# Kernel optimization log

Hardware: AMD Instinct MI355X
Metric: run time of the kernel (lower is better)

Reference implementation:

```python
import jax, jax.numpy as jnp
import numpy as np

N = 27          # num_classes (nodes)
C = 512         # in_channels
B = 64          # batch
EPS = 1e-5


def _bn(x, gamma, beta):
    # BatchNorm1d over [b, channels, feat]: normalize over (batch, feat), training mode (batch stats, biased var)
    mean = jnp.mean(x, axis=(0, 2), keepdims=True)
    var = jnp.mean((x - mean) ** 2, axis=(0, 2), keepdims=True)
    return gamma[None, :, None] * (x - mean) * jax.lax.rsqrt(var + EPS) + beta[None, :, None]


def _layer(x, edge, WA, WB, WE, WU, WV, ge, be, gv, bv):
    # x: [b, n, c], edge: [b, n*n, c]; edge index e = i*n + j; end[e,i]=1, start[e,j]=1
    b = x.shape[0]
    res = x
    Vix = x @ WA.T                       # [b, n, c]  (gathered to edges via end)
    Vjx = x @ WB.T                       # [b, n, c]  (gathered to edges via start)
    e_lin = edge @ WE.T                  # [b, n*n, c]
    # einsum('ev,bvc->bec', end, Vix) == broadcast Vix over j; start gathers Vjx over i
    msg = (Vix[:, :, None, :] + Vjx[:, None, :, :]).reshape(b, N * N, C) + e_lin
    edge = edge + jax.nn.relu(_bn(msg, ge, be))
    # attention: sigmoid then softmax over j (dim 2 of [b, n, n, c])
    e = jax.nn.sigmoid(edge).reshape(b, N, N, C)
    e = jax.nn.softmax(e, axis=2).reshape(b, N * N, C)
    Ujx = x @ WV.T                       # [b, n, c], gathered via start -> broadcast over i
    Ujx_e = jnp.broadcast_to(Ujx[:, None, :, :], (b, N, N, C)).reshape(b, N * N, C)
    Uix = x @ WU.T
    # einsum('ve,bec->bvc', end.T, t) == sum over j of t[b, i*n+j]
    agg = (e * Ujx_e).reshape(b, N, N, C).sum(axis=2)
    x = Uix + agg / N
    x = jax.nn.relu(res + _bn(x, gv, bv))
    return x, edge


def setup_inputs() -> dict:
    key = jax.random.key(0)
    ks = jax.random.split(key, 12)
    scale = np.sqrt(2.0 / C)
    w = lambda k: (jax.random.normal(k, (C, C), dtype=jnp.float32) * scale)
    inp = {
        "x": jax.random.normal(ks[0], (B, N, C), dtype=jnp.float32),
        "edge": jax.random.normal(ks[1], (B, N * N, C), dtype=jnp.float32),
        "WU1": w(ks[2]), "WV1": w(ks[3]), "WA1": w(ks[4]), "WB1": w(ks[5]), "WE1": w(ks[6]),
        "WU2": w(ks[7]), "WV2": w(ks[8]), "WA2": w(ks[9]), "WB2": w(ks[10]), "WE2": w(ks[11]),
        "gv1": jnp.ones((N,), jnp.float32), "bv1": jnp.zeros((N,), jnp.float32),
        "ge1": jnp.ones((N * N,), jnp.float32), "be1": jnp.zeros((N * N,), jnp.float32),
        "gv2": jnp.ones((N,), jnp.float32), "bv2": jnp.zeros((N,), jnp.float32),
        "ge2": jnp.ones((N * N,), jnp.float32), "be2": jnp.zeros((N * N,), jnp.float32),
    }
    return inp


def reference(x, edge, WU1, WV1, WA1, WB1, WE1, WU2, WV2, WA2, WB2, WE2,
              gv1, bv1, ge1, be1, gv2, bv2, ge2, be2):
    x, edge = _layer(x, edge, WA1, WB1, WE1, WU1, WV1, ge1, be1, gv1, bv1)
    x, edge = _layer(x, edge, WA2, WB2, WE2, WU2, WV2, ge2, be2, gv2, bv2)
    return x, edge
```

## Files before the change

kernel.cpp:

```cpp
#include <hip/hip_runtime.h>

typedef unsigned short u16;
typedef unsigned int u32;
typedef __bf16 bf16x8 __attribute__((ext_vector_type(8)));
typedef float f32x4 __attribute__((ext_vector_type(4)));

#define DI __device__ __forceinline__

DI u16 f2bf(float f) {
  union { float f; u32 u; } v; v.f = f;
  return (u16)((v.u + 0x7fffu + ((v.u >> 16) & 1u)) >> 16);
}
DI float bf2f(u16 h) {
  union { u32 u; float f; } v; v.u = ((u32)h) << 16;
  return v.f;
}

DI void gload_lds16(const void* g, void* l) {
  __builtin_amdgcn_global_load_lds((const __attribute__((address_space(1))) u32*)g,
                                   (__attribute__((address_space(3))) u32*)l, 16, 0, 0);
}

constexpr float INV_M = 1.0f / 32768.0f;

__global__ void convw_k(const float* wa1, const float* wb1, const float* wu1, const float* wv1, const float* we1,
                        const float* wa2, const float* wb2, const float* wu2, const float* wv2, const float* we2,
                        u16* dst) {
  int idx = blockIdx.x * 256 + threadIdx.x;
  int m = idx >> 16;
  int i = (idx & 0xffff) << 2;
  const float* s;
  switch (m) {
    case 0: s = wa1; break; case 1: s = wb1; break; case 2: s = wu1; break;
    case 3: s = wv1; break; case 4: s = we1; break; case 5: s = wa2; break;
    case 6: s = wb2; break; case 7: s = wu2; break; case 8: s = wv2; break;
    default: s = we2; break;
  }
  float4 v = *(const float4*)(s + i);
  ushort4 o;
  o.x = f2bf(v.x); o.y = f2bf(v.y); o.z = f2bf(v.z); o.w = f2bf(v.w);
  *(ushort4*)(dst + ((size_t)m << 18) + i) = o;
}

template<int EPI, int ABF, int SWZ, int NT>
__global__ __launch_bounds__(256, 5) void gemm_k(
    const void* __restrict__ A_, const u16* __restrict__ W,
    float* __restrict__ outf, int ldout,
    u16* __restrict__ msg, const float* __restrict__ V4,
    float* __restrict__ esum, float* __restrict__ esq) {
  __shared__ __align__(16) u16 lA[64 * 64];
  __shared__ __align__(16) u16 lW[32 * NT * 64];
  const int tid = threadIdx.x;
  const int lane = tid & 63, wid = tid >> 6;
  const int wm = wid >> 1, wn = wid & 1;
  const int q = lane >> 4, l15 = lane & 15;
  const int lrow8 = lane >> 3, lg = lane & 7;

  int rb, cb;
  if (SWZ) {
    int l = blockIdx.x;
    int xcd = l & 7, t = l >> 3;
    cb = t & 3;
    rb = ((t >> 2) << 3) | xcd;
    if (rb >= 729) return;
  } else {
    rb = blockIdx.y; cb = blockIdx.x;
  }

  f32x4 acc[2][NT];
#pragma unroll
  for (int a = 0; a < 2; a++)
#pragma unroll
    for (int b = 0; b < NT; b++) acc[a][b] = (f32x4){0.f, 0.f, 0.f, 0.f};

  for (int k0 = 0; k0 < 512; k0 += 64) {
    __syncthreads();
    if (ABF) {
#pragma unroll
      for (int it = 0; it < 2; it++) {
        int ch = wid * 2 + it;
        int row = ch * 8 + lrow8;
        const u16* src = (const u16*)A_ + (((size_t)(rb * 64 + row)) << 9) + k0 + ((lg ^ (row & 7)) << 3);
        gload_lds16(src, lA + ch * 512);
      }
    } else {
#pragma unroll
      for (int s = tid; s < 512; s += 256) {
        int row = s >> 3, g = s & 7;
        const float* src = (const float*)A_ + (((size_t)(rb * 64 + row)) << 9) + k0 + g * 8;
        float4 s0 = *(const float4*)src;
        float4 s1 = *(const float4*)(src + 4);
        uint4 p;
        p.x = f2bf(s0.x) | ((u32)f2bf(s0.y) << 16);
        p.y = f2bf(s0.z) | ((u32)f2bf(s0.w) << 16);
        p.z = f2bf(s1.x) | ((u32)f2bf(s1.y) << 16);
        p.w = f2bf(s1.z) | ((u32)f2bf(s1.w) << 16);
        *(uint4*)(lA + row * 64 + ((g ^ (row & 7)) << 3)) = p;
      }
    }
#pragma unroll
    for (int it = 0; it < NT; it++) {
      int ch = wid * NT + it;
      int row = ch * 8 + lrow8;
      const u16* src = W + (((size_t)(cb * 32 * NT + row)) << 9) + k0 + ((lg ^ (row & 7)) << 3);
      gload_lds16(src, lW + ch * 512);
    }
    __syncthreads();
#pragma unroll
    for (int ks = 0; ks < 2; ks++) {
      const int gk = ks * 4 + q;
      bf16x8 af[2], wf[NT];
#pragma unroll
      for (int mt = 0; mt < 2; mt++) {
        int r = wm * 32 + mt * 16 + l15;
        af[mt] = *(const bf16x8*)(lA + r * 64 + ((gk ^ (r & 7)) << 3));
      }
#pragma unroll
      for (int nt = 0; nt < NT; nt++) {
        int r = wn * 16 * NT + nt * 16 + l15;
        wf[nt] = *(const bf16x8*)(lW + r * 64 + ((gk ^ (r & 7)) << 3));
      }
#pragma unroll
      for (int mt = 0; mt < 2; mt++)
#pragma unroll
        for (int nt = 0; nt < NT; nt++)
          acc[mt][nt] = __builtin_amdgcn_mfma_f32_16x16x32_bf16(af[mt], wf[nt], acc[mt][nt], 0, 0, 0);
    }
  }

  if (EPI == 1) {
#pragma unroll
    for (int mt = 0; mt < 2; mt++) {
      int grow0 = rb * 64 + wm * 32 + mt * 16 + q * 4;
#pragma unroll
      for (int nt = 0; nt < NT; nt++) {
        int gcol = cb * 32 * NT + wn * 16 * NT + nt * 16 + l15;
#pragma unroll
        for (int r = 0; r < 4; r++)
          outf[(size_t)(grow0 + r) * ldout + gcol] = acc[mt][nt][r];
      }
    }
  } else {
    float ms[2][4], m2[2][4];
#pragma unroll
    for (int mt = 0; mt < 2; mt++) {
#pragma unroll
      for (int r = 0; r < 4; r++) {
        int grow = rb * 64 + wm * 32 + mt * 16 + q * 4 + r;
        int b = grow / 729;
        int e = grow - b * 729;
        int i = e / 27;
        int j = e - i * 27;
        const float* vix = V4 + (((size_t)(b * 27 + i)) << 11);
        const float* vjx = V4 + (((size_t)(b * 27 + j)) << 11) + 512;
        u16* mrow = msg + (((size_t)grow) << 9);
        float s1 = 0.f, s2 = 0.f;
#pragma unroll
        for (int nt = 0; nt < NT; nt++) {
          int c = cb * 32 * NT + wn * 16 * NT + nt * 16 + l15;
          float m = acc[mt][nt][r] + vix[c] + vjx[c];
          mrow[c] = f2bf(m);
          s1 += m;
          s2 += m * m;
        }
        ms[mt][r] = s1;
        m2[mt][r] = s2;
      }
    }
#pragma unroll
    for (int msk = 1; msk < 16; msk <<= 1) {
#pragma unroll
      for (int mt = 0; mt < 2; mt++)
#pragma unroll
        for (int r = 0; r < 4; r++) {
          ms[mt][r] += __shfl_xor(ms[mt][r], msk);
          m2[mt][r] += __shfl_xor(m2[mt][r], msk);
        }
    }
    __syncthreads();
    float* sm = (float*)lA;
    if (l15 == 0) {
#pragma unroll
      for (int mt = 0; mt < 2; mt++)
#pragma unroll
        for (int r = 0; r < 4; r++) {
          int rib = wm * 32 + mt * 16 + q * 4 + r;
          sm[wn * 64 + rib] = ms[mt][r];
          sm[128 + wn * 64 + rib] = m2[mt][r];
        }
    }
    __syncthreads();
    if (tid < 64) {
      int grow = rb * 64 + tid;
      int e = grow % 729;
      atomicAdd(&esum[e], sm[tid] + sm[64 + tid]);
      atomicAdd(&esq[e], sm[128 + tid] + sm[192 + tid]);
    }
  }
}

template<int INBF, int OUTBF>
__global__ __launch_bounds__(256) void edge_attn_k(
    const u16* __restrict__ msg, const void* __restrict__ ein_, void* __restrict__ eout_,
    const float* __restrict__ esum, const float* __restrict__ esq,
    const float* __restrict__ ge, const float* __restrict__ be,
    const float* __restrict__ V4,
    float* __restrict__ xnew, float* __restrict__ vsum, float* __restrict__ vsq) {
  const int bi = blockIdx.x;
  const int b = bi / 27, i = bi - b * 27;
  const int t = threadIdx.x;
  __shared__ float2 sab[27];
  if (t < 27) {
    int e = i * 27 + t;
    float mean = esum[e] * INV_M;
    float var = esq[e] * INV_M - mean * mean;
    float a = ge[e] * rsqrtf(var + 1e-5f);
    sab[t] = make_float2(a, be[e] - mean * a);
  }
  __syncthreads();
  const size_t ebase = (((size_t)(b * 729 + i * 27)) << 9) + 2 * t;
  const u16* einb = (const u16*)ein_;
  const float* einf = (const float*)ein_;
  u16* eoutb = (u16*)eout_;
  float* eoutf = (float*)eout_;
  float t0[27], t1[27];
  float ss0 = 0.f, ss1 = 0.f;
#pragma unroll
  for (int j = 0; j < 27; j++) {
    size_t idx = ebase + (((size_t)j) << 9);
    float2 ab = sab[j];
    u32 mp = *(const u32*)(msg + idx);
    float2 ei;
    if (INBF) {
      u32 ep = *(const u32*)(einb + idx);
      ei = make_float2(bf2f((u16)ep), bf2f((u16)(ep >> 16)));
    } else {
      ei = *(const float2*)(einf + idx);
    }
    float e0 = ei.x + fmaxf(fmaf(ab.x, bf2f((u16)mp), ab.y), 0.f);
    float e1 = ei.y + fmaxf(fmaf(ab.x, bf2f((u16)(mp >> 16)), ab.y), 0.f);
    if (OUTBF) {
      *(u32*)(eoutb + idx) = (u32)f2bf(e0) | ((u32)f2bf(e1) << 16);
    } else {
      *(float2*)(eoutf + idx) = make_float2(e0, e1);
    }
    float x0 = __expf(1.f / (1.f + __expf(-e0)));
    float x1 = __expf(1.f / (1.f + __expf(-e1)));
    ss0 += x0; ss1 += x1;
    t0[j] = x0; t1[j] = x1;
  }
  float a0 = 0.f, a1 = 0.f;
#pragma unroll
  for (int j = 0; j < 27; j++) {
    float2 uj = *(const float2*)(V4 + (((size_t)(b * 27 + j)) << 11) + 1536 + 2 * t);
    a0 = fmaf(t0[j], uj.x, a0);
    a1 = fmaf(t1[j], uj.y, a1);
  }
  float2 ui = *(const float2*)(V4 + (((size_t)(b * 27 + i)) << 11) + 1024 + 2 * t);
  float xn0 = ui.x + a0 / (ss0 * 27.f);
  float xn1 = ui.y + a1 / (ss1 * 27.f);
  *(float2*)(xnew + (((size_t)bi) << 9) + 2 * t) = make_float2(xn0, xn1);
  float v = xn0 + xn1, v2 = xn0 * xn0 + xn1 * xn1;
#pragma unroll
  for (int m = 32; m >= 1; m >>= 1) {
    v += __shfl_xor(v, m);
    v2 += __shfl_xor(v2, m);
  }
  __shared__ float red[8];
  int w = t >> 6, ln = t & 63;
  if (ln == 0) { red[w] = v; red[4 + w] = v2; }
  __syncthreads();
  if (t == 0) {
    float s1 = 0.f, s2 = 0.f;
#pragma unroll
    for (int k = 0; k < 4; k++) { s1 += red[k]; s2 += red[4 + k]; }
    atomicAdd(&vsum[i], s1);
    atomicAdd(&vsq[i], s2);
  }
}

__global__ void vert_bn_k(const float4* __restrict__ xnew, const float4* __restrict__ res,
                          const float* __restrict__ vsum, const float* __restrict__ vsq,
                          const float* __restrict__ g, const float* __restrict__ bt,
                          float4* __restrict__ out) {
  int idx = blockIdx.x * 256 + threadIdx.x;
  int i = (idx >> 7) % 27;
  float mean = vsum[i] * INV_M;
  float var = vsq[i] * INV_M - mean * mean;
  float a = g[i] * rsqrtf(var + 1e-5f);
  float bb = bt[i] - mean * a;
  float4 xv = xnew[idx];
  float4 rv = res[idx];
  float4 o;
  o.x = fmaxf(rv.x + fmaf(a, xv.x, bb), 0.f);
  o.y = fmaxf(rv.y + fmaf(a, xv.y, bb), 0.f);
  o.z = fmaxf(rv.z + fmaf(a, xv.z, bb), 0.f);
  o.w = fmaxf(rv.w + fmaf(a, xv.w, bb), 0.f);
  out[idx] = o;
}

extern "C" void kernel_launch(void* const* d_in, const int* in_sizes, int n_in,
                              void* d_out, int out_size, void* d_ws, size_t ws_size,
                              hipStream_t stream) {
  const float* x    = (const float*)d_in[0];
  const float* edge = (const float*)d_in[1];
  const float* WU1 = (const float*)d_in[2];
  const float* WV1 = (const float*)d_in[3];
  const float* WA1 = (const float*)d_in[4];
  const float* WB1 = (const float*)d_in[5];
  const float* WE1 = (const float*)d_in[6];
  const float* WU2 = (const float*)d_in[7];
  const float* WV2 = (const float*)d_in[8];
  const float* WA2 = (const float*)d_in[9];
  const float* WB2 = (const float*)d_in[10];
  const float* WE2 = (const float*)d_in[11];
  const float* gv1 = (const float*)d_in[12];
  const float* bv1 = (const float*)d_in[13];
  const float* ge1 = (const float*)d_in[14];
  const float* be1 = (const float*)d_in[15];
  const float* gv2 = (const float*)d_in[16];
  const float* bv2 = (const float*)d_in[17];
  const float* ge2 = (const float*)d_in[18];
  const float* be2 = (const float*)d_in[19];

  char* ws = (char*)d_ws;
  u16*   wbf  = (u16*)(ws + 0);
  float* V4   = (float*)(ws + 5242880);
  u16*   M1   = (u16*)(ws + 19398656);
  u16*   M2   = (u16*)(ws + 67174400);
  float* xnew = (float*)(ws + 114950144);
  float* x1   = (float*)(ws + 118489088);
  float* st   = (float*)(ws + 122028032);
  float* es1 = st;         float* eq1 = st + 729;
  float* es2 = st + 1458;  float* eq2 = st + 2187;
  float* vs1 = st + 2916;  float* vq1 = st + 2943;
  float* vs2 = st + 2970;  float* vq2 = st + 2997;

  float* xout = (float*)d_out;
  float* eo   = (float*)d_out + 884736;

  hipMemsetAsync(st, 0, 3024 * sizeof(float), stream);
  convw_k<<<dim3(2560), dim3(256), 0, stream>>>(WA1, WB1, WU1, WV1, WE1, WA2, WB2, WU2, WV2, WE2, wbf);

  gemm_k<1, 0, 0, 2><<<dim3(32, 27), dim3(256), 0, stream>>>(x, wbf, V4, 2048, nullptr, nullptr, nullptr, nullptr);
  gemm_k<2, 0, 1, 4><<<dim3(2944), dim3(256), 0, stream>>>(edge, wbf + 4 * 262144, nullptr, 0, M1, V4, es1, eq1);
  edge_attn_k<0, 1><<<dim3(1728), dim3(256), 0, stream>>>(M1, edge, M1, es1, eq1, ge1, be1, V4, xnew, vs1, vq1);
  vert_bn_k<<<dim3(864), dim3(256), 0, stream>>>((const float4*)xnew, (const float4*)x, vs1, vq1, gv1, bv1, (float4*)x1);

  gemm_k<1, 0, 0, 2><<<dim3(32, 27), dim3(256), 0, stream>>>(x1, wbf + 5 * 262144, V4, 2048, nullptr, nullptr, nullptr, nullptr);
  gemm_k<2, 1, 1, 4><<<dim3(2944), dim3(256), 0, stream>>>(M1, wbf + 9 * 262144, nullptr, 0, M2, V4, es2, eq2);
  edge_attn_k<1, 0><<<dim3(1728), dim3(256), 0, stream>>>(M2, M1, eo, es2, eq2, ge2, be2, V4, xnew, vs2, vq2);
  vert_bn_k<<<dim3(864), dim3(256), 0, stream>>>((const float4*)xnew, (const float4*)x1, vs2, vq2, gv2, bv2, (float4*)xout);
}
```

Baseline: 442.0 us.

## Replace LDS-staged GEMM with direct register-fragment loads and prefetch

The GEMM kernel no longer stages A and W tiles through shared memory. Each wave now loads its MFMA fragments straight from global memory into registers and double-buffers them, prefetching the next k-slice while the current MFMAs run. Every wave owns a 32x64 sub-tile, and the vertex GEMM grid is halved to match a 128-column block. This removes the LDS traffic and the per-k-step barriers, but each wave fetches its own copy of data that other waves share, with less coalesced global access and more register pressure.

```diff
diff --git a/kernel.cpp b/kernel.cpp
--- a/kernel.cpp
+++ b/kernel.cpp
@@ -15,10 +15,13 @@
   union { u32 u; float f; } v; v.u = ((u32)h) << 16;
   return v.f;
 }
-
-DI void gload_lds16(const void* g, void* l) {
-  __builtin_amdgcn_global_load_lds((const __attribute__((address_space(1))) u32*)g,
-                                   (__attribute__((address_space(3))) u32*)l, 16, 0, 0);
+DI bf16x8 pack8(float4 a, float4 b) {
+  union { bf16x8 v; u32 u[4]; } r;
+  r.u[0] = (u32)f2bf(a.x) | ((u32)f2bf(a.y) << 16);
+  r.u[1] = (u32)f2bf(a.z) | ((u32)f2bf(a.w) << 16);
+  r.u[2] = (u32)f2bf(b.x) | ((u32)f2bf(b.y) << 16);
+  r.u[3] = (u32)f2bf(b.z) | ((u32)f2bf(b.w) << 16);
+  return r.v;
 }
 
 constexpr float INV_M = 1.0f / 32768.0f;
@@ -42,20 +45,16 @@
   *(ushort4*)(dst + ((size_t)m << 18) + i) = o;
 }
 
-template<int EPI, int ABF, int SWZ, int NT>
-__global__ __launch_bounds__(256, 5) void gemm_k(
+template<int EPI, int ABF, int SWZ>
+__global__ __launch_bounds__(256, 4) void gemm_k(
     const void* __restrict__ A_, const u16* __restrict__ W,
     float* __restrict__ outf, int ldout,
     u16* __restrict__ msg, const float* __restrict__ V4,
     float* __restrict__ esum, float* __restrict__ esq) {
-  __shared__ __align__(16) u16 lA[64 * 64];
-  __shared__ __align__(16) u16 lW[32 * NT * 64];
   const int tid = threadIdx.x;
   const int lane = tid & 63, wid = tid >> 6;
-  const int wm = wid >> 1, wn = wid & 1;
+  const int vm = wid & 1, vn = wid >> 1;
   const int q = lane >> 4, l15 = lane & 15;
-  const int lrow8 = lane >> 3, lg = lane & 7;
-
   int rb, cb;
   if (SWZ) {
     int l = blockIdx.x;
@@ -67,86 +66,92 @@
     rb = blockIdx.y; cb = blockIdx.x;
   }
 
-  f32x4 acc[2][NT];
+  const u16*   wp0 = W + ((size_t)(cb * 128 + vn * 64 + l15) << 9) + q * 8;
+  const u16*   ab0 = (const u16*)A_  + ((size_t)(rb * 64 + vm * 32 + l15) << 9) + q * 8;
+  const float* af0 = (const float*)A_ + ((size_t)(rb * 64 + vm * 32 + l15) << 9) + q * 8;
+
+  f32x4 acc[2][4];
 #pragma unroll
   for (int a = 0; a < 2; a++)
 #pragma unroll
-    for (int b = 0; b < NT; b++) acc[a][b] = (f32x4){0.f, 0.f, 0.f, 0.f};
-
-  for (int k0 = 0; k0 < 512; k0 += 64) {
-    __syncthreads();
-    if (ABF) {
-#pragma unroll
-      for (int it = 0; it < 2; it++) {
-        int ch = wid * 2 + it;
-        int row = ch * 8 + lrow8;
-        const u16* src = (const u16*)A_ + (((size_t)(rb * 64 + row)) << 9) + k0 + ((lg ^ (row & 7)) << 3);
-        gload_lds16(src, lA + ch * 512);
+    for (int b = 0; b < 4; b++) acc[a][b] = (f32x4){0.f, 0.f, 0.f, 0.f};
+
+  bf16x8 wc[4], wn_[4];
+  bf16x8 ac[2], an_[2];
+  float4 fc[2][2], fn[2][2];
+
+#pragma unroll
+  for (int nt = 0; nt < 4; nt++) wc[nt] = *(const bf16x8*)(wp0 + nt * 8192);
+  if (ABF) {
+#pragma unroll
+    for (int mt = 0; mt < 2; mt++) ac[mt] = *(const bf16x8*)(ab0 + mt * 8192);
+  } else {
+#pragma unroll
+    for (int mt = 0; mt < 2; mt++) {
+      fc[mt][0] = *(const float4*)(af0 + mt * 8192);
+      fc[mt][1] = *(const float4*)(af0 + mt * 8192 + 4);
+    }
+  }
+
+#pragma unroll
+  for (int ks = 0; ks < 16; ks++) {
+    if (ks < 15) {
+      const int ko = (ks + 1) * 32;
+#pragma unroll
+      for (int nt = 0; nt < 4; nt++) wn_[nt] = *(const bf16x8*)(wp0 + nt * 8192 + ko);
+      if (ABF) {
+#pragma unroll
+        for (int mt = 0; mt < 2; mt++) an_[mt] = *(const bf16x8*)(ab0 + mt * 8192 + ko);
+      } else {
+#pragma unroll
+        for (int mt = 0; mt < 2; mt++) {
+          fn[mt][0] = *(const float4*)(af0 + mt * 8192 + ko);
+          fn[mt][1] = *(const float4*)(af0 + mt * 8192 + ko + 4);
+        }
       }
-    } else {
-#pragma unroll
-      for (int s = tid; s < 512; s += 256) {
-        int row = s >> 3, g = s & 7;
-        const float* src = (const float*)A_ + (((size_t)(rb * 64 + row)) << 9) + k0 + g * 8;
-        float4 s0 = *(const float4*)src;
-        float4 s1 = *(const float4*)(src + 4);
-        uint4 p;
-        p.x = f2bf(s0.x) | ((u32)f2bf(s0.y) << 16);
-        p.y = f2bf(s0.z) | ((u32)f2bf(s0.w) << 16);
-        p.z = f2bf(s1.x) | ((u32)f2bf(s1.y) << 16);
-        p.w = f2bf(s1.z) | ((u32)f2bf(s1.w) << 16);
-        *(uint4*)(lA + row * 64 + ((g ^ (row & 7)) << 3)) = p;
+    }
+    bf16x8 afr[2];
+#pragma unroll
+    for (int mt = 0; mt < 2; mt++)
+      afr[mt] = ABF ? ac[mt] : pack8(fc[mt][0], fc[mt][1]);
+#pragma unroll
+    for (int mt = 0; mt < 2; mt++)
+#pragma unroll
+      for (int nt = 0; nt < 4; nt++)
+        acc[mt][nt] = __builtin_amdgcn_mfma_f32_16x16x32_bf16(afr[mt], wc[nt], acc[mt][nt], 0, 0, 0);
+    if (ks < 15) {
+#pragma unroll
+      for (int nt = 0; nt < 4; nt++) wc[nt] = wn_[nt];
+      if (ABF) {
+#pragma unroll
+        for (int mt = 0; mt < 2; mt++) ac[mt] = an_[mt];
+      } else {
+#pragma unroll
+        for (int mt = 0; mt < 2; mt++) { fc[mt][0] = fn[mt][0]; fc[mt][1] = fn[mt][1]; }
       }
     }
-#pragma unroll
-    for (int it = 0; it < NT; it++) {
-      int ch = wid * NT + it;
-      int row = ch * 8 + lrow8;
-      const u16* src = W + (((size_t)(cb * 32 * NT + row)) << 9) + k0 + ((lg ^ (row & 7)) << 3);
-      gload_lds16(src, lW + ch * 512);
-    }
-    __syncthreads();
-#pragma unroll
-    for (int ks = 0; ks < 2; ks++) {
-      const int gk = ks * 4 + q;
-      bf16x8 af[2], wf[NT];
-#pragma unroll
-      for (int mt = 0; mt < 2; mt++) {
-        int r = wm * 32 + mt * 16 + l15;
-        af[mt] = *(const bf16x8*)(lA + r * 64 + ((gk ^ (r & 7)) << 3));
-      }
-#pragma unroll
-      for (int nt = 0; nt < NT; nt++) {
-        int r = wn * 16 * NT + nt * 16 + l15;
-        wf[nt] = *(const bf16x8*)(lW + r * 64 + ((gk ^ (r & 7)) << 3));
-      }
-#pragma unroll
-      for (int mt = 0; mt < 2; mt++)
-#pragma unroll
-        for (int nt = 0; nt < NT; nt++)
-          acc[mt][nt] = __builtin_amdgcn_mfma_f32_16x16x32_bf16(af[mt], wf[nt], acc[mt][nt], 0, 0, 0);
-    }
   }
 
   if (EPI == 1) {
 #pragma unroll
     for (int mt = 0; mt < 2; mt++) {
-      int grow0 = rb * 64 + wm * 32 + mt * 16 + q * 4;
-#pragma unroll
-      for (int nt = 0; nt < NT; nt++) {
-        int gcol = cb * 32 * NT + wn * 16 * NT + nt * 16 + l15;
+      int grow0 = rb * 64 + vm * 32 + mt * 16 + q * 4;
+#pragma unroll
+      for (int nt = 0; nt < 4; nt++) {
+        int gcol = cb * 128 + vn * 64 + nt * 16 + l15;
 #pragma unroll
         for (int r = 0; r < 4; r++)
           outf[(size_t)(grow0 + r) * ldout + gcol] = acc[mt][nt][r];
       }
     }
   } else {
+    __shared__ float sm[256];
     float ms[2][4], m2[2][4];
 #pragma unroll
     for (int mt = 0; mt < 2; mt++) {
 #pragma unroll
       for (int r = 0; r < 4; r++) {
-        int grow = rb * 64 + wm * 32 + mt * 16 + q * 4 + r;
+        int grow = rb * 64 + vm * 32 + mt * 16 + q * 4 + r;
         int b = grow / 729;
         int e = grow - b * 729;
         int i = e / 27;
@@ -156,8 +161,8 @@
         u16* mrow = msg + (((size_t)grow) << 9);
         float s1 = 0.f, s2 = 0.f;
 #pragma unroll
-        for (int nt = 0; nt < NT; nt++) {
-          int c = cb * 32 * NT + wn * 16 * NT + nt * 16 + l15;
+        for (int nt = 0; nt < 4; nt++) {
+          int c = cb * 128 + vn * 64 + nt * 16 + l15;
           float m = acc[mt][nt][r] + vix[c] + vjx[c];
           mrow[c] = f2bf(m);
           s1 += m;
@@ -178,15 +183,14 @@
         }
     }
     __syncthreads();
-    float* sm = (float*)lA;
     if (l15 == 0) {
 #pragma unroll
       for (int mt = 0; mt < 2; mt++)
 #pragma unroll
         for (int r = 0; r < 4; r++) {
-          int rib = wm * 32 + mt * 16 + q * 4 + r;
-          sm[wn * 64 + rib] = ms[mt][r];
-          sm[128 + wn * 64 + rib] = m2[mt][r];
+          int rib = vm * 32 + mt * 16 + q * 4 + r;
+          sm[vn * 64 + rib] = ms[mt][r];
+          sm[128 + vn * 64 + rib] = m2[mt][r];
         }
     }
     __syncthreads();
@@ -342,13 +346,13 @@
   hipMemsetAsync(st, 0, 3024 * sizeof(float), stream);
   convw_k<<<dim3(2560), dim3(256), 0, stream>>>(WA1, WB1, WU1, WV1, WE1, WA2, WB2, WU2, WV2, WE2, wbf);
 
-  gemm_k<1, 0, 0, 2><<<dim3(32, 27), dim3(256), 0, stream>>>(x, wbf, V4, 2048, nullptr, nullptr, nullptr, nullptr);
-  gemm_k<2, 0, 1, 4><<<dim3(2944), dim3(256), 0, stream>>>(edge, wbf + 4 * 262144, nullptr, 0, M1, V4, es1, eq1);
+  gemm_k<1, 0, 0><<<dim3(16, 27), dim3(256), 0, stream>>>(x, wbf, V4, 2048, nullptr, nullptr, nullptr, nullptr);
+  gemm_k<2, 0, 1><<<dim3(2944), dim3(256), 0, stream>>>(edge, wbf + 4 * 262144, nullptr, 0, M1, V4, es1, eq1);
   edge_attn_k<0, 1><<<dim3(1728), dim3(256), 0, stream>>>(M1, edge, M1, es1, eq1, ge1, be1, V4, xnew, vs1, vq1);
   vert_bn_k<<<dim3(864), dim3(256), 0, stream>>>((const float4*)xnew, (const float4*)x, vs1, vq1, gv1, bv1, (float4*)x1);
 
-  gemm_k<1, 0, 0, 2><<<dim3(32, 27), dim3(256), 0, stream>>>(x1, wbf + 5 * 262144, V4, 2048, nullptr, nullptr, nullptr, nullptr);
-  gemm_k<2, 1, 1, 4><<<dim3(2944), dim3(256), 0, stream>>>(M1, wbf + 9 * 262144, nullptr, 0, M2, V4, es2, eq2);
+  gemm_k<1, 0, 0><<<dim3(16, 27), dim3(256), 0, stream>>>(x1, wbf + 5 * 262144, V4, 2048, nullptr, nullptr, nullptr, nullptr);
+  gemm_k<2, 1, 1><<<dim3(2944), dim3(256), 0, stream>>>(M1, wbf + 9 * 262144, nullptr, 0, M2, V4, es2, eq2);
   edge_attn_k<1, 0><<<dim3(1728), dim3(256), 0, stream>>>(M2, M1, eo, es2, eq2, ge2, be2, V4, xnew, vs2, vq2);
   vert_bn_k<<<dim3(864), dim3(256), 0, stream>>>((const float4*)xnew, (const float4*)x1, vs2, vq2, gv2, bv2, (float4*)xout);
 }
```

After: 668.1 us. +51.1%, slower.

## Double-buffer weight tiles and register-prefetch A tiles in GEMM main loop

Applied to the files above, without the earlier changes.

Restructures the GEMM K-loop into a software pipeline. The next K-tile of W is loaded asynchronously into a second LDS buffer, and the next A tile is prefetched into registers while the MFMAs run on the current tile. The A registers are written to LDS after a barrier. This hides global-load latency behind compute, at the cost of extra LDS and registers, so launch bounds drop from 5 to 4 blocks per CU. The bf16 A path now also goes through registers instead of direct global-to-LDS loads.

```diff
diff --git a/kernel.cpp b/kernel.cpp
--- a/kernel.cpp
+++ b/kernel.cpp
@@ -43,18 +43,19 @@
 }
 
 template<int EPI, int ABF, int SWZ, int NT>
-__global__ __launch_bounds__(256, 5) void gemm_k(
+__global__ __launch_bounds__(256, 4) void gemm_k(
     const void* __restrict__ A_, const u16* __restrict__ W,
     float* __restrict__ outf, int ldout,
     u16* __restrict__ msg, const float* __restrict__ V4,
     float* __restrict__ esum, float* __restrict__ esq) {
   __shared__ __align__(16) u16 lA[64 * 64];
-  __shared__ __align__(16) u16 lW[32 * NT * 64];
+  __shared__ __align__(16) u16 lW[2][32 * NT * 64];
   const int tid = threadIdx.x;
   const int lane = tid & 63, wid = tid >> 6;
   const int wm = wid >> 1, wn = wid & 1;
   const int q = lane >> 4, l15 = lane & 15;
   const int lrow8 = lane >> 3, lg = lane & 7;
+  const int arow = tid >> 3, ag = tid & 7;
 
   int rb, cb;
   if (SWZ) {
@@ -67,45 +68,72 @@
     rb = blockIdx.y; cb = blockIdx.x;
   }
 
+  float4 pAf[2][2];
+  uint4 pAb[2];
+
+#define ISSUE_W(buf, k0)                                                                            \
+  {                                                                                                 \
+    _Pragma("unroll")                                                                               \
+    for (int it = 0; it < NT; it++) {                                                               \
+      int ch = wid * NT + it;                                                                       \
+      int row = ch * 8 + lrow8;                                                                     \
+      const u16* src = W + (((size_t)(cb * 32 * NT + row)) << 9) + (k0) + ((lg ^ (row & 7)) << 3);  \
+      gload_lds16(src, &lW[buf][ch * 512]);                                                         \
+    }                                                                                               \
+  }
+
+#define LOAD_A(k0)                                                                                  \
+  {                                                                                                 \
+    if (ABF) {                                                                                      \
+      _Pragma("unroll")                                                                             \
+      for (int i = 0; i < 2; i++)                                                                   \
+        pAb[i] = *(const uint4*)((const u16*)A_ + (((size_t)(rb * 64 + arow + 32 * i)) << 9) + (k0) + (ag << 3)); \
+    } else {                                                                                        \
+      _Pragma("unroll")                                                                             \
+      for (int i = 0; i < 2; i++) {                                                                 \
+        const float* s = (const float*)A_ + (((size_t)(rb * 64 + arow + 32 * i)) << 9) + (k0) + (ag << 3); \
+        pAf[i][0] = *(const float4*)s;                                                              \
+        pAf[i][1] = *(const float4*)(s + 4);                                                        \
+      }                                                                                             \
+    }                                                                                               \
+  }
+
+#define WRITE_A()                                                                                   \
+  {                                                                                                 \
+    _Pragma("unroll")                                                                               \
+    for (int i = 0; i < 2; i++) {                                                                   \
+      int row = arow + 32 * i;                                                                      \
+      uint4 p;                                                                                      \
+      if (ABF) {                                                                                    \
+        p = pAb[i];                                                                                 \
+      } else {                                                                                      \
+        p.x = f2bf(pAf[i][0].x) | ((u32)f2bf(pAf[i][0].y) << 16);                                   \
+        p.y = f2bf(pAf[i][0].z) | ((u32)f2bf(pAf[i][0].w) << 16);                                   \
+        p.z = f2bf(pAf[i][1].x) | ((u32)f2bf(pAf[i][1].y) << 16);                                   \
+        p.w = f2bf(pAf[i][1].z) | ((u32)f2bf(pAf[i][1].w) << 16);                                   \
+      }                                                                                             \
+      *(uint4*)(lA + row * 64 + ((ag ^ (row & 7)) << 3)) = p;                                       \
+    }                                                                                               \
+  }
+
   f32x4 acc[2][NT];
 #pragma unroll
   for (int a = 0; a < 2; a++)
 #pragma unroll
     for (int b = 0; b < NT; b++) acc[a][b] = (f32x4){0.f, 0.f, 0.f, 0.f};
 
-  for (int k0 = 0; k0 < 512; k0 += 64) {
+  LOAD_A(0);
+  ISSUE_W(0, 0);
+  WRITE_A();
+
+#pragma unroll 2
+  for (int kt = 0; kt < 8; kt++) {
     __syncthreads();
-    if (ABF) {
-#pragma unroll
-      for (int it = 0; it < 2; it++) {
-        int ch = wid * 2 + it;
-        int row = ch * 8 + lrow8;
-        const u16* src = (const u16*)A_ + (((size_t)(rb * 64 + row)) << 9) + k0 + ((lg ^ (row & 7)) << 3);
-        gload_lds16(src, lA + ch * 512);
-      }
-    } else {
-#pragma unroll
-      for (int s = tid; s < 512; s += 256) {
-        int row = s >> 3, g = s & 7;
-        const float* src = (const float*)A_ + (((size_t)(rb * 64 + row)) << 9) + k0 + g * 8;
-        float4 s0 = *(const float4*)src;
-        float4 s1 = *(const float4*)(src + 4);
-        uint4 p;
-        p.x = f2bf(s0.x) | ((u32)f2bf(s0.y) << 16);
-        p.y = f2bf(s0.z) | ((u32)f2bf(s0.w) << 16);
-        p.z = f2bf(s1.x) | ((u32)f2bf(s1.y) << 16);
-        p.w = f2bf(s1.z) | ((u32)f2bf(s1.w) << 16);
-        *(uint4*)(lA + row * 64 + ((g ^ (row & 7)) << 3)) = p;
-      }
-    }
-#pragma unroll
-    for (int it = 0; it < NT; it++) {
-      int ch = wid * NT + it;
-      int row = ch * 8 + lrow8;
-      const u16* src = W + (((size_t)(cb * 32 * NT + row)) << 9) + k0 + ((lg ^ (row & 7)) << 3);
-      gload_lds16(src, lW + ch * 512);
-    }
-    __syncthreads();
+    if (kt < 7) {
+      ISSUE_W((kt + 1) & 1, (kt + 1) * 64);
+      LOAD_A((kt + 1) * 64);
+    }
+    const u16* lWc = lW[kt & 1];
 #pragma unroll
     for (int ks = 0; ks < 2; ks++) {
       const int gk = ks * 4 + q;
@@ -118,7 +146,7 @@
 #pragma unroll
       for (int nt = 0; nt < NT; nt++) {
         int r = wn * 16 * NT + nt * 16 + l15;
-        wf[nt] = *(const bf16x8*)(lW + r * 64 + ((gk ^ (r & 7)) << 3));
+        wf[nt] = *(const bf16x8*)(lWc + r * 64 + ((gk ^ (r & 7)) << 3));
       }
 #pragma unroll
       for (int mt = 0; mt < 2; mt++)
@@ -126,6 +154,8 @@
         for (int nt = 0; nt < NT; nt++)
           acc[mt][nt] = __builtin_amdgcn_mfma_f32_16x16x32_bf16(af[mt], wf[nt], acc[mt][nt], 0, 0, 0);
     }
+    __syncthreads();
+    if (kt < 7) WRITE_A();
   }
 
   if (EPI == 1) {
```

New measurement: 432.3 us. -2.2%, faster.

## Double-buffer GEMM tiles via register prefetch and split edge attention over channels

Applied to the files above, without the earlier changes.

The GEMM drops direct global-to-LDS loads in favour of register-staged prefetch two k-tiles ahead into double-buffered LDS, with one barrier per k-step, so global loads overlap MFMA work. Occupancy hint drops from 5 to 3 waves because of the higher register and LDS use. The node GEMM switches to NT=4 with half the column blocks. Edge attention launches twice as many blocks, each thread handling one channel instead of two, which raises parallelism but makes memory accesses narrower.

```diff
diff --git a/kernel.cpp b/kernel.cpp
--- a/kernel.cpp
+++ b/kernel.cpp
@@ -15,10 +15,13 @@
   union { u32 u; float f; } v; v.u = ((u32)h) << 16;
   return v.f;
 }
-
-DI void gload_lds16(const void* g, void* l) {
-  __builtin_amdgcn_global_load_lds((const __attribute__((address_space(1))) u32*)g,
-                                   (__attribute__((address_space(3))) u32*)l, 16, 0, 0);
+DI uint4 packu4(const float4& a, const float4& b) {
+  uint4 p;
+  p.x = (u32)f2bf(a.x) | ((u32)f2bf(a.y) << 16);
+  p.y = (u32)f2bf(a.z) | ((u32)f2bf(a.w) << 16);
+  p.z = (u32)f2bf(b.x) | ((u32)f2bf(b.y) << 16);
+  p.w = (u32)f2bf(b.z) | ((u32)f2bf(b.w) << 16);
+  return p;
 }
 
 constexpr float INV_M = 1.0f / 32768.0f;
@@ -43,18 +46,18 @@
 }
 
 template<int EPI, int ABF, int SWZ, int NT>
-__global__ __launch_bounds__(256, 5) void gemm_k(
+__global__ __launch_bounds__(256, 3) void gemm_k(
     const void* __restrict__ A_, const u16* __restrict__ W,
     float* __restrict__ outf, int ldout,
     u16* __restrict__ msg, const float* __restrict__ V4,
     float* __restrict__ esum, float* __restrict__ esq) {
-  __shared__ __align__(16) u16 lA[64 * 64];
-  __shared__ __align__(16) u16 lW[32 * NT * 64];
+  __shared__ __align__(16) u16 lA[2][64 * 64];
+  __shared__ __align__(16) u16 lW[2][32 * NT * 64];
   const int tid = threadIdx.x;
   const int lane = tid & 63, wid = tid >> 6;
   const int wm = wid >> 1, wn = wid & 1;
   const int q = lane >> 4, l15 = lane & 15;
-  const int lrow8 = lane >> 3, lg = lane & 7;
+  const int arow = tid >> 3, ag = tid & 7;
 
   int rb, cb;
   if (SWZ) {
@@ -67,45 +70,62 @@
     rb = blockIdx.y; cb = blockIdx.x;
   }
 
+  float4 sAf[2][2][2];
+  uint4 sAb[2][2];
+  uint4 sW[2][NT];
+
+#define LOADR(st, k0)                                                                              \
+  {                                                                                                \
+    if (ABF) {                                                                                     \
+      _Pragma("unroll")                                                                            \
+      for (int i = 0; i < 2; i++)                                                                  \
+        sAb[st][i] = *(const uint4*)((const u16*)A_ + (((size_t)(rb * 64 + arow + 32 * i)) << 9) + (k0) + ag * 8); \
+    } else {                                                                                       \
+      _Pragma("unroll")                                                                            \
+      for (int i = 0; i < 2; i++) {                                                                \
+        const float* s_ = (const float*)A_ + (((size_t)(rb * 64 + arow + 32 * i)) << 9) + (k0) + ag * 8; \
+        sAf[st][i][0] = *(const float4*)s_;                                                        \
+        sAf[st][i][1] = *(const float4*)(s_ + 4);                                                  \
+      }                                                                                            \
+    }                                                                                              \
+    _Pragma("unroll")                                                                              \
+    for (int it = 0; it < NT; it++) {                                                              \
+      int row = it * 32 + arow;                                                                    \
+      sW[st][it] = *(const uint4*)(W + (((size_t)(cb * 32 * NT + row)) << 9) + (k0) + ag * 8);     \
+    }                                                                                              \
+  }
+
+#define WRITEL(st, buf)                                                                            \
+  {                                                                                                \
+    _Pragma("unroll")                                                                              \
+    for (int i = 0; i < 2; i++) {                                                                  \
+      int row = arow + 32 * i;                                                                     \
+      uint4 p = ABF ? sAb[st][i] : packu4(sAf[st][i][0], sAf[st][i][1]);                           \
+      *(uint4*)(&lA[buf][row * 64 + ((ag ^ (row & 7)) << 3)]) = p;                                 \
+    }                                                                                              \
+    _Pragma("unroll")                                                                              \
+    for (int it = 0; it < NT; it++) {                                                              \
+      int row = it * 32 + arow;                                                                    \
+      *(uint4*)(&lW[buf][row * 64 + ((ag ^ (row & 7)) << 3)]) = sW[st][it];                        \
+    }                                                                                              \
+  }
+
   f32x4 acc[2][NT];
 #pragma unroll
   for (int a = 0; a < 2; a++)
 #pragma unroll
     for (int b = 0; b < NT; b++) acc[a][b] = (f32x4){0.f, 0.f, 0.f, 0.f};
 
-  for (int k0 = 0; k0 < 512; k0 += 64) {
+  LOADR(0, 0);
+  LOADR(1, 64);
+  WRITEL(0, 0);
+
+#pragma unroll
+  for (int kt = 0; kt < 8; kt++) {
     __syncthreads();
-    if (ABF) {
-#pragma unroll
-      for (int it = 0; it < 2; it++) {
-        int ch = wid * 2 + it;
-        int row = ch * 8 + lrow8;
-        const u16* src = (const u16*)A_ + (((size_t)(rb * 64 + row)) << 9) + k0 + ((lg ^ (row & 7)) << 3);
-        gload_lds16(src, lA + ch * 512);
-      }
-    } else {
-#pragma unroll
-      for (int s = tid; s < 512; s += 256) {
-        int row = s >> 3, g = s & 7;
-        const float* src = (const float*)A_ + (((size_t)(rb * 64 + row)) << 9) + k0 + g * 8;
-        float4 s0 = *(const float4*)src;
-        float4 s1 = *(const float4*)(src + 4);
-        uint4 p;
-        p.x = f2bf(s0.x) | ((u32)f2bf(s0.y) << 16);
-        p.y = f2bf(s0.z) | ((u32)f2bf(s0.w) << 16);
-        p.z = f2bf(s1.x) | ((u32)f2bf(s1.y) << 16);
-        p.w = f2bf(s1.z) | ((u32)f2bf(s1.w) << 16);
-        *(uint4*)(lA + row * 64 + ((g ^ (row & 7)) << 3)) = p;
-      }
-    }
-#pragma unroll
-    for (int it = 0; it < NT; it++) {
-      int ch = wid * NT + it;
-      int row = ch * 8 + lrow8;
-      const u16* src = W + (((size_t)(cb * 32 * NT + row)) << 9) + k0 + ((lg ^ (row & 7)) << 3);
-      gload_lds16(src, lW + ch * 512);
-    }
-    __syncthreads();
+    if (kt + 2 < 8) LOADR(kt & 1, (kt + 2) * 64);
+    const u16* lAc = lA[kt & 1];
+    const u16* lWc = lW[kt & 1];
 #pragma unroll
     for (int ks = 0; ks < 2; ks++) {
       const int gk = ks * 4 + q;
@@ -113,12 +133,12 @@
 #pragma unroll
       for (int mt = 0; mt < 2; mt++) {
         int r = wm * 32 + mt * 16 + l15;
-        af[mt] = *(const bf16x8*)(lA + r * 64 + ((gk ^ (r & 7)) << 3));
+        af[mt] = *(const bf16x8*)(lAc + r * 64 + ((gk ^ (r & 7)) << 3));
       }
 #pragma unroll
       for (int nt = 0; nt < NT; nt++) {
         int r = wn * 16 * NT + nt * 16 + l15;
-        wf[nt] = *(const bf16x8*)(lW + r * 64 + ((gk ^ (r & 7)) << 3));
+        wf[nt] = *(const bf16x8*)(lWc + r * 64 + ((gk ^ (r & 7)) << 3));
       }
 #pragma unroll
       for (int mt = 0; mt < 2; mt++)
@@ -126,6 +146,7 @@
         for (int nt = 0; nt < NT; nt++)
           acc[mt][nt] = __builtin_amdgcn_mfma_f32_16x16x32_bf16(af[mt], wf[nt], acc[mt][nt], 0, 0, 0);
     }
+    if (kt + 1 < 8) WRITEL((kt + 1) & 1, (kt + 1) & 1);
   }
 
   if (EPI == 1) {
@@ -206,74 +227,56 @@
     const float* __restrict__ ge, const float* __restrict__ be,
     const float* __restrict__ V4,
     float* __restrict__ xnew, float* __restrict__ vsum, float* __restrict__ vsq) {
-  const int bi = blockIdx.x;
+  const int blk = blockIdx.x;
+  const int bi = blk >> 1;
   const int b = bi / 27, i = bi - b * 27;
-  const int t = threadIdx.x;
+  const int c = ((blk & 1) << 8) + threadIdx.x;
   __shared__ float2 sab[27];
-  if (t < 27) {
-    int e = i * 27 + t;
+  if (threadIdx.x < 27) {
+    int e = i * 27 + threadIdx.x;
     float mean = esum[e] * INV_M;
     float var = esq[e] * INV_M - mean * mean;
     float a = ge[e] * rsqrtf(var + 1e-5f);
-    sab[t] = make_float2(a, be[e] - mean * a);
+    sab[threadIdx.x] = make_float2(a, be[e] - mean * a);
   }
   __syncthreads();
-  const size_t ebase = (((size_t)(b * 729 + i * 27)) << 9) + 2 * t;
+  const size_t ebase = (((size_t)(b * 729 + i * 27)) << 9) + c;
   const u16* einb = (const u16*)ein_;
   const float* einf = (const float*)ein_;
   u16* eoutb = (u16*)eout_;
   float* eoutf = (float*)eout_;
-  float t0[27], t1[27];
-  float ss0 = 0.f, ss1 = 0.f;
+  float texp[27];
+  float ssum = 0.f;
 #pragma unroll
   for (int j = 0; j < 27; j++) {
     size_t idx = ebase + (((size_t)j) << 9);
     float2 ab = sab[j];
-    u32 mp = *(const u32*)(msg + idx);
-    float2 ei;
-    if (INBF) {
-      u32 ep = *(const u32*)(einb + idx);
-      ei = make_float2(bf2f((u16)ep), bf2f((u16)(ep >> 16)));
-    } else {
-      ei = *(const float2*)(einf + idx);
-    }
-    float e0 = ei.x + fmaxf(fmaf(ab.x, bf2f((u16)mp), ab.y), 0.f);
-    float e1 = ei.y + fmaxf(fmaf(ab.x, bf2f((u16)(mp >> 16)), ab.y), 0.f);
-    if (OUTBF) {
-      *(u32*)(eoutb + idx) = (u32)f2bf(e0) | ((u32)f2bf(e1) << 16);
-    } else {
-      *(float2*)(eoutf + idx) = make_float2(e0, e1);
-    }
-    float x0 = __expf(1.f / (1.f + __expf(-e0)));
-    float x1 = __expf(1.f / (1.f + __expf(-e1)));
-    ss0 += x0; ss1 += x1;
-    t0[j] = x0; t1[j] = x1;
-  }
-  float a0 = 0.f, a1 = 0.f;
-#pragma unroll
-  for (int j = 0; j < 27; j++) {
-    float2 uj = *(const float2*)(V4 + (((size_t)(b * 27 + j)) << 11) + 1536 + 2 * t);
-    a0 = fmaf(t0[j], uj.x, a0);
-    a1 = fmaf(t1[j], uj.y, a1);
-  }
-  float2 ui = *(const float2*)(V4 + (((size_t)(b * 27 + i)) << 11) + 1024 + 2 * t);
-  float xn0 = ui.x + a0 / (ss0 * 27.f);
-  float xn1 = ui.y + a1 / (ss1 * 27.f);
-  *(float2*)(xnew + (((size_t)bi) << 9) + 2 * t) = make_float2(xn0, xn1);
-  float v = xn0 + xn1, v2 = xn0 * xn0 + xn1 * xn1;
+    float ei = INBF ? bf2f(einb[idx]) : einf[idx];
+    float eo = ei + fmaxf(fmaf(ab.x, bf2f(msg[idx]), ab.y), 0.f);
+    if (OUTBF) eoutb[idx] = f2bf(eo); else eoutf[idx] = eo;
+    float t = __expf(1.f / (1.f + __expf(-eo)));
+    ssum += t;
+    texp[j] = t;
+  }
+  float accv = 0.f;
+#pragma unroll
+  for (int j = 0; j < 27; j++)
+    accv = fmaf(texp[j], V4[(((size_t)(b * 27 + j)) << 11) + 1536 + c], accv);
+  float xn = V4[(((size_t)(b * 27 + i)) << 11) + 1024 + c] + accv / (ssum * 27.f);
+  xnew[(((size_t)bi) << 9) + c] = xn;
+  float v = xn, v2 = xn * xn;
 #pragma unroll
   for (int m = 32; m >= 1; m >>= 1) {
     v += __shfl_xor(v, m);
     v2 += __shfl_xor(v2, m);
   }
   __shared__ float red[8];
-  int w = t >> 6, ln = t & 63;
+  int w = threadIdx.x >> 6, ln = threadIdx.x & 63;
   if (ln == 0) { red[w] = v; red[4 + w] = v2; }
   __syncthreads();
-  if (t == 0) {
-    float s1 = 0.f, s2 = 0.f;
-#pragma unroll
-    for (int k = 0; k < 4; k++) { s1 += red[k]; s2 += red[4 + k]; }
+  if (threadIdx.x == 0) {
+    float s1 = red[0] + red[1] + red[2] + red[3];
+    float s2 = red[4] + red[5] + red[6] + red[7];
     atomicAdd(&vsum[i], s1);
     atomicAdd(&vsq[i], s2);
   }
@@ -342,13 +345,13 @@
   hipMemsetAsync(st, 0, 3024 * sizeof(float), stream);
   convw_k<<<dim3(2560), dim3(256), 0, stream>>>(WA1, WB1, WU1, WV1, WE1, WA2, WB2, WU2, WV2, WE2, wbf);
 
-  gemm_k<1, 0, 0, 2><<<dim3(32, 27), dim3(256), 0, stream>>>(x, wbf, V4, 2048, nullptr, nullptr, nullptr, nullptr);
+  gemm_k<1, 0, 0, 4><<<dim3(16, 27), dim3(256), 0, stream>>>(x, wbf, V4, 2048, nullptr, nullptr, nullptr, nullptr);
   gemm_k<2, 0, 1, 4><<<dim3(2944), dim3(256), 0, stream>>>(edge, wbf + 4 * 262144, nullptr, 0, M1, V4, es1, eq1);
-  edge_attn_k<0, 1><<<dim3(1728), dim3(256), 0, stream>>>(M1, edge, M1, es1, eq1, ge1, be1, V4, xnew, vs1, vq1);
+  edge_attn_k<0, 1><<<dim3(3456), dim3(256), 0, stream>>>(M1, edge, M1, es1, eq1, ge1, be1, V4, xnew, vs1, vq1);
   vert_bn_k<<<dim3(864), dim3(256), 0, stream>>>((const float4*)xnew, (const float4*)x, vs1, vq1, gv1, bv1, (float4*)x1);
 
-  gemm_k<1, 0, 0, 2><<<dim3(32, 27), dim3(256), 0, stream>>>(x1, wbf + 5 * 262144, V4, 2048, nullptr, nullptr, nullptr, nullptr);
+  gemm_k<1, 0, 0, 4><<<dim3(16, 27), dim3(256), 0, stream>>>(x1, wbf + 5 * 262144, V4, 2048, nullptr, nullptr, nullptr, nullptr);
   gemm_k<2, 1, 1, 4><<<dim3(2944), dim3(256), 0, stream>>>(M1, wbf + 9 * 262144, nullptr, 0, M2, V4, es2, eq2);
-  edge_attn_k<1, 0><<<dim3(1728), dim3(256), 0, stream>>>(M2, M1, eo, es2, eq2, ge2, be2, V4, xnew, vs2, vq2);
+  edge_attn_k<1, 0><<<dim3(3456), dim3(256), 0, stream>>>(M2, M1, eo, es2, eq2, ge2, be2, V4, xnew, vs2, vq2);
   vert_bn_k<<<dim3(864), dim3(256), 0, stream>>>((const float4*)xnew, (const float4*)x1, vs2, vq2, gv2, bv2, (float4*)xout);
 }
```

Result: slower. 672.8 us (+52.2%).
